# Kernel optimization log

Measured on AMD Instinct MI355X. Metric: run time of the kernel, lower is better.

Reference implementation:

```python
import jax, jax.numpy as jnp
import numpy as np

DN = ('NCHW', 'OIHW', 'NCHW')
EPS = 1e-5

def _conv(x, w, stride, padding):
    return jax.lax.conv_general_dilated(x, w, stride, padding, dimension_numbers=DN)

def _bn(x, g, b, m, v):
    # inference-mode BatchNorm2d
    s = g * jax.lax.rsqrt(v + EPS)
    return x * s[None, :, None, None] + (b - m * s)[None, :, None, None]

def _gn(x, g, b, groups):
    B, C, H, W = x.shape
    xr = x.reshape(B, groups, -1)
    mu = xr.mean(axis=2, keepdims=True)
    var = xr.var(axis=2, keepdims=True)
    xn = ((xr - mu) * jax.lax.rsqrt(var + EPS)).reshape(B, C, H, W)
    return xn * g[None, :, None, None] + b[None, :, None, None]

def _dsconv(f, ow, ob, og, obb, om, ov, w, wb, gg, gb, morph, k=3, extend_scope=1.0):
    B, C, H, W = f.shape
    S = H  # source DSC coordinate map only type-checks for square inputs
    off = jnp.tanh(_bn(_conv(f, ow, (1, 1), [(1, 1), (1, 1)]) + ob[None, :, None, None], og, obb, om, ov))
    # source passes y_offset for morph 0, x_offset for morph 1; both are added to y_new
    sel = off[:, :k] if morph == 0 else off[:, k:]
    center = k // 2
    # _apply_offset: detached clone, center zeroed; cumulative loop is empty for k=3
    off_cum = jax.lax.stop_gradient(sel).at[:, center].set(0.0) * extend_scope
    vals = jnp.linspace(float((-k) // 2), float(k // 2), k, dtype=f.dtype)  # [-2,-0.5,1] for k=3 (source quirk)
    rowc = jnp.arange(S, dtype=f.dtype)[:, None]  # both y_center and x_center equal the row index
    yg = jnp.zeros((k,), f.dtype) if morph == 0 else vals
    xg = vals if morph == 0 else jnp.zeros((k,), f.dtype)
    y = rowc[None, None] + yg[None, :, None, None] + off_cum                       # (B,k,S,S)
    x = jnp.broadcast_to(rowc[None, None] + xg[None, :, None, None], (B, k, S, S))
    rs = lambda t: t.transpose(0, 2, 1, 3).reshape(B, k * S, S)  # b p w h -> b (w p) h
    y, x = rs(y), rs(x)
    y0 = jnp.clip(jnp.floor(y), 0, S - 1); y1 = jnp.clip(jnp.floor(y) + 1.0, 0, S - 1)
    x0 = jnp.clip(jnp.floor(x), 0, S - 1); x1 = jnp.clip(jnp.floor(x) + 1.0, 0, S - 1)
    # source: index_a0 = base_y0 - base + x0  (batch offset cancels -> all batches gather from batch 0)
    flat0 = f[0].transpose(1, 2, 0).reshape(S * S, C)
    gat = lambda yy, xx: flat0[(yy * S + xx).astype(jnp.int32)]  # (B,kS,S,C)
    out = (gat(y0, x0) * ((y1 - y) * (x1 - x))[..., None]
         + gat(y0, x1) * ((y1 - y) * (x - x0))[..., None]
         + gat(y1, x0) * ((y - y0) * (x1 - x))[..., None]
         + gat(y1, x1) * ((y - y0) * (x - x0))[..., None])
    if morph == 0:
        df = out.transpose(0, 3, 1, 2)                    # (B,C,k*S,S)
        z = _conv(df, w, (k, 1), 'VALID')
    else:
        df = out.reshape(B, S, k * S, C).transpose(0, 3, 1, 2)  # (B,C,S,k*S)
        z = _conv(df, w, (1, k), 'VALID')
    z = z + wb[None, :, None, None]
    return jax.nn.silu(_gn(z, gg, gb, w.shape[0] // 4))

def _forward(x, w0, g0, b0, m0, v0,
             owx, obx, ogx, obbx, omx, ovx, wx, bwx, ggx, gbx,
             owy, oby, ogy, obby, omy, ovy, wy, bwy, ggy, gby):
    out0 = jax.nn.silu(_bn(_conv(x, w0, (1, 1), [(1, 1), (1, 1)]), g0, b0, m0, v0))
    outx = _dsconv(x, owx, obx, ogx, obbx, omx, ovx, wx, bwx, ggx, gbx, morph=0)
    outy = _dsconv(x, owy, oby, ogy, obby, omy, ovy, wy, bwy, ggy, gby, morph=1)
    return jnp.concatenate([out0, outx, outy], axis=1)

def setup_inputs() -> dict:
    B, C, O, S, K = 4, 64, 64, 256, 3
    key = jax.random.key(0)
    ks = jax.random.split(key, 32)
    rn = lambda i, sh, sc=1.0: jax.random.normal(ks[i], sh, dtype=jnp.float32) * sc
    ru = lambda i, sh: jax.random.uniform(ks[i], sh, dtype=jnp.float32) + 0.5
    return {
        'x': rn(0, (B, C, S, S)),
        'w0': rn(1, (O, C, 3, 3), 0.05), 'g0': ru(2, (O,)), 'b0': rn(3, (O,), 0.1),
        'm0': rn(4, (O,), 0.1), 'v0': ru(5, (O,)),
        'owx': rn(6, (2 * K, C, 3, 3), 0.05), 'obx': rn(7, (2 * K,), 0.1),
        'ogx': ru(8, (2 * K,)), 'obbx': rn(9, (2 * K,), 0.1), 'omx': rn(10, (2 * K,), 0.1), 'ovx': ru(11, (2 * K,)),
        'wx': rn(12, (O, C, K, 1), 0.05), 'bwx': rn(13, (O,), 0.1), 'ggx': ru(14, (O,)), 'gbx': rn(15, (O,), 0.1),
        'owy': rn(16, (2 * K, C, 3, 3), 0.05), 'oby': rn(17, (2 * K,), 0.1),
        'ogy': ru(18, (2 * K,)), 'obby': rn(19, (2 * K,), 0.1), 'omy': rn(20, (2 * K,), 0.1), 'ovy': ru(21, (2 * K,)),
        'wy': rn(22, (O, C, 1, K), 0.05), 'bwy': rn(23, (O,), 0.1), 'ggy': ru(24, (O,)), 'gby': rn(25, (O,), 0.1),
    }

def reference(x, w0, g0, b0, m0, v0,
              owx, obx, ogx, obbx, omx, ovx, wx, bwx, ggx, gbx,
              owy, oby, ogy, obby, omy, ovy, wy, bwy, ggy, gby):
    return _forward(x, w0, g0, b0, m0, v0,
                    owx, obx, ogx, obbx, omx, ovx, wx, bwx, ggx, gbx,
                    owy, oby, ogy, obby, omy, ovy, wy, bwy, ggy, gby)
```

## Files before the change

### kernel.cpp

```cpp
#include <hip/hip_runtime.h>
#include <hip/hip_bf16.h>
#include <math.h>

#define TS 256
#define HW 65536
#define CIN 64
#define EPSV 1e-5f
#define XPITCH 258

typedef __attribute__((ext_vector_type(8))) short bf16x8;
typedef __attribute__((ext_vector_type(4))) float f32x4;
typedef __attribute__((ext_vector_type(16))) float f32x16;
typedef __attribute__((ext_vector_type(4))) unsigned short u16x4;
typedef unsigned short ushort_t;

__device__ __forceinline__ float silu_f(float v){ return v / (1.0f + expf(-v)); }
__device__ __forceinline__ ushort_t f2bf(float f){
    __hip_bfloat16 h = __float2bfloat16(f);
    return *reinterpret_cast<ushort_t*>(&h);
}
__device__ __forceinline__ float bf2f(ushort_t u){
    unsigned int t = ((unsigned int)u) << 16;
    return __uint_as_float(t);
}

__global__ __launch_bounds__(256) void k_xbf(const float* __restrict__ x, ushort_t* __restrict__ xbf){
    int blk = blockIdx.x;
    int tid = threadIdx.x;
    if (blk < 4096){
        __shared__ float tile[64][65];
        int b = blk >> 10;
        int chunk = blk & 1023;
        int p0 = chunk * 64;
        int i = p0 >> 8, jb = p0 & 255;
        int lane = tid & 63, grp = tid >> 6;
        #pragma unroll
        for (int k = 0; k < 16; ++k){
            int c = k*4 + grp;
            tile[lane][c] = x[((size_t)(b*CIN + c))*HW + p0 + lane];
        }
        __syncthreads();
        #pragma unroll
        for (int k = 0; k < 16; ++k){
            int pp = k*4 + grp;
            xbf[(((size_t)b*258 + (i+1))*XPITCH + 1 + jb + pp)*64 + lane] = f2bf(tile[pp][lane]);
        }
    } else {
        int base = (blk - 4096) * 1024;
        #pragma unroll
        for (int k = 0; k < 4; ++k){
            int h = base + k*256 + tid;
            if (h < 132096){
                int b = h / 33024;
                int rem = h - b*33024;
                int r = (rem >= 16512) ? 257 : 0;
                int e = (rem >= 16512) ? rem - 16512 : rem;
                xbf[((size_t)b*258 + r)*XPITCH*64 + e] = 0;
            } else if (h < 263168){
                int h2 = h - 132096;
                int b = h2 >> 15;
                int rem = h2 & 32767;
                int row = rem >> 7;
                int rem2 = rem & 127;
                int colsel = rem2 >> 6;
                int c = rem2 & 63;
                xbf[(((size_t)b*258 + row + 1)*XPITCH + (colsel ? 257 : 0))*64 + c] = 0;
            }
        }
    }
}

__global__ __launch_bounds__(256) void k_wpack(const float* __restrict__ w0,
        const float* __restrict__ wx, const float* __restrict__ wy,
        ushort_t* __restrict__ w0bf, ushort_t* __restrict__ wbfx, ushort_t* __restrict__ wbfy){
    int idx = blockIdx.x*256 + threadIdx.x;
    if (idx < 36864){
        int r = idx >> 12;
        int rem = idx & 4095;
        int o = rem >> 6, c = rem & 63;
        w0bf[idx] = f2bf(w0[(o*64 + c)*9 + r]);
    } else {
        int k2 = idx - 36864;
        int set = k2 / 12288;
        int rem = k2 - set*12288;
        int o = rem / 192;
        int k = rem - o*192;
        int t = k >> 6, c = k & 63;
        const float* w = set ? wy : wx;
        ushort_t* dst = set ? wbfy : wbfx;
        dst[rem] = f2bf(w[(o*64 + c)*3 + t]);
    }
}

__global__ __launch_bounds__(256) void k_offp(const float* __restrict__ x,
        const float* __restrict__ owx, const float* __restrict__ owy,
        float* __restrict__ poff){
    __shared__ float xs[8][4][258];
    __shared__ float wsm[4][8][9];
    int by = blockIdx.y;
    int b = by >> 3, chunk = by & 7;
    int i0 = blockIdx.x * 2;
    int tid = threadIdx.x;
    for (int idx = tid; idx < 4*8*9; idx += 256){
        int o = idx / 72;
        int rem = idx - o*72;
        int c = rem / 9, tap = rem - c*9;
        int morph = o >> 1;
        int ch = (o==0)?0:(o==1)?2:(o==2)?3:5;
        const float* w = morph ? owy : owx;
        wsm[o][c][tap] = w[(ch*64 + chunk*8 + c)*9 + tap];
    }
    for (int idx = tid; idx < 8*4*258; idx += 256){
        int c = idx / 1032;
        int rem = idx - c*1032;
        int rr = rem / 258, col = rem - rr*258;
        int gy = i0 + rr - 1, gx = col - 1;
        float v = 0.f;
        if (gy >= 0 && gy < 256 && gx >= 0 && gx < 256)
            v = x[((size_t)(b*64 + chunk*8 + c))*HW + gy*256 + gx];
        xs[c][rr][col] = v;
    }
    __syncthreads();
    float acc[4][2];
    #pragma unroll
    for (int o = 0; o < 4; ++o){ acc[o][0]=0.f; acc[o][1]=0.f; }
    int j = tid;
    #pragma unroll
    for (int c = 0; c < 8; ++c){
        float vrow[4][3];
        #pragma unroll
        for (int rr = 0; rr < 4; ++rr){
            vrow[rr][0] = xs[c][rr][j];
            vrow[rr][1] = xs[c][rr][j+1];
            vrow[rr][2] = xs[c][rr][j+2];
        }
        #pragma unroll
        for (int o = 0; o < 4; ++o){
            const float* wr = wsm[o][c];
            #pragma unroll
            for (int ky = 0; ky < 3; ++ky){
                #pragma unroll
                for (int kx = 0; kx < 3; ++kx){
                    float wv = wr[ky*3+kx];
                    acc[o][0] += wv * vrow[ky][kx];
                    acc[o][1] += wv * vrow[ky+1][kx];
                }
            }
        }
    }
    #pragma unroll
    for (int o = 0; o < 4; ++o){
        size_t base = ((size_t)((chunk*4 + o)*4 + b))*HW;
        poff[base + (size_t)i0*256 + j]     = acc[o][0];
        poff[base + (size_t)(i0+1)*256 + j] = acc[o][1];
    }
}

__global__ __launch_bounds__(256) void k_mid(
        const ushort_t* __restrict__ xbf, const ushort_t* __restrict__ w0bf,
        const float* __restrict__ g0, const float* __restrict__ b0,
        const float* __restrict__ m0, const float* __restrict__ v0,
        const float* __restrict__ poff,
        const float* __restrict__ ogx, const float* __restrict__ ovx,
        const float* __restrict__ obx, const float* __restrict__ omx,
        const float* __restrict__ obbx,
        const float* __restrict__ ogy, const float* __restrict__ ovy,
        const float* __restrict__ oby, const float* __restrict__ omy,
        const float* __restrict__ obby,
        float* __restrict__ off0, float* __restrict__ off1,
        float* __restrict__ out){
    __shared__ __align__(16) ushort_t Xs[3*130*64];
    int blk = blockIdx.x;
    int tid = threadIdx.x;
    if (blk < 2048){
        int id2 = ((blk & 7) << 8) + (blk >> 3);
        int b  = id2 >> 9;
        int i  = (id2 >> 1) & 255;
        int jh = id2 & 1;
        int j0h = jh*128;
        int wv = tid >> 6;
        int lane = tid & 63;
        int l31 = lane & 31;
        int kh = lane >> 5;
        int obase = (wv & 1) * 32;
        int pxb = (wv >> 1) * 64;

        for (int idx = tid; idx < 3120; idx += 256){
            int rr = idx / 1040;
            int rem = idx - rr*1040;
            int p = rem >> 3, cgrp = rem & 7;
            bf16x8 v = *(const bf16x8*)(xbf + (((size_t)b*258 + (i + rr))*XPITCH + j0h + p)*64 + cgrp*8);
            int byte = rr*16640 + p*128 + ((cgrp*16) ^ ((p & 7) << 4));
            *(bf16x8*)((char*)Xs + byte) = v;
        }
        __syncthreads();

        f32x16 acc0, acc1;
        #pragma unroll
        for (int e = 0; e < 16; ++e){ acc0[e] = 0.f; acc1[e] = 0.f; }

        #pragma unroll
        for (int r = 0; r < 9; ++r){
            const int rr = r/3, dx = r%3 - 1;
            bf16x8 af[4];
            #pragma unroll
            for (int kg = 0; kg < 4; ++kg)
                af[kg] = *(const bf16x8*)(w0bf + (size_t)r*4096 + (obase + l31)*64 + kg*16 + kh*8);
            #pragma unroll
            for (int kg = 0; kg < 4; ++kg){
                int cb = kg*32 + kh*16;
                int p0_ = pxb + l31 + dx + 1;
                bf16x8 b0_ = *(const bf16x8*)((char*)Xs + rr*16640 + p0_*128 + (cb ^ ((p0_ & 7) << 4)));
                acc0 = __builtin_amdgcn_mfma_f32_32x32x16_bf16(af[kg], b0_, acc0, 0, 0, 0);
                int p1_ = p0_ + 32;
                bf16x8 b1_ = *(const bf16x8*)((char*)Xs + rr*16640 + p1_*128 + (cb ^ ((p1_ & 7) << 4)));
                acc1 = __builtin_amdgcn_mfma_f32_32x32x16_bf16(af[kg], b1_, acc1, 0, 0, 0);
            }
        }
        #pragma unroll
        for (int reg = 0; reg < 16; ++reg){
            int o = obase + (reg & 3) + 8*(reg >> 2) + 4*kh;
            float s = g0[o] * rsqrtf(v0[o] + EPSV);
            float bi = b0[o] - m0[o]*s;
            int j = j0h + pxb + l31;
            out[((size_t)(b*192 + o))*HW + i*TS + j]      = silu_f(acc0[reg]*s + bi);
            out[((size_t)(b*192 + o))*HW + i*TS + j + 32] = silu_f(acc1[reg]*s + bi);
        }
    } else {
        int idx = (blk - 2048)*256 + tid;
        int px = idx & 65535;
        int t2 = idx >> 16;
        int b = t2 & 3;
        int o6 = t2 >> 2;
        float s_ = 0.f;
        #pragma unroll
        for (int chunk = 0; chunk < 8; ++chunk)
            s_ += poff[((size_t)((chunk*4 + o6)*4 + b))*HW + px];
        int morph = o6 >> 1;
        int ch = (o6==0)?0:(o6==1)?2:(o6==2)?3:5;
        const float* og_ = morph? ogy:ogx; const float* ov_ = morph? ovy:ovx;
        const float* ob_ = morph? oby:obx; const float* om_ = morph? omy:omx;
        const float* obb_ = morph? obby:obbx;
        float sc = og_[ch]*rsqrtf(ov_[ch]+EPSV);
        float bi = (ob_[ch]-om_[ch])*sc + obb_[ch];
        int pl = (o6 & 1)*2;
        float* dst = (morph? off1:off0) + ((size_t)(b*3+pl))*HW;
        dst[px] = tanhf(s_*sc + bi);
    }
}

__global__ __launch_bounds__(256) void k_dsc2m(const ushort_t* __restrict__ xbf,
        const float* __restrict__ off0, const float* __restrict__ off1,
        const ushort_t* __restrict__ wbfx, const ushort_t* __restrict__ wbfy,
        const float* __restrict__ bwx, const float* __restrict__ bwy,
        ushort_t* __restrict__ zbuf, float* __restrict__ part){
    __shared__ __align__(16) ushort_t Vt[3*64*64];
    __shared__ __align__(16) ushort_t Xg[7][4][64];
    int mz = blockIdx.z;
    int b = mz & 3;
    int morph = mz >> 2;
    int i = blockIdx.y;
    int j0 = blockIdx.x * 64;
    int tid = threadIdx.x;
    int lane16 = tid & 15;
    int pq = tid >> 4;
    const float fi = (float)i;
    const float* offm = morph ? off1 : off0;

    if (morph == 0){
        int vec = tid >> 4;
        int s = vec >> 2, cs = vec & 3;
        int row = min(max(i - 1 + s, 0), 255);
        int col = min(max(i - 2 + cs, 0), 255);
        *(u16x4*)&Xg[s][cs][lane16*4] =
            *(const u16x4*)(xbf + ((size_t)(row+1)*XPITCH + 1 + col)*64 + lane16*4);
    } else {
        if (tid < 112){
            int s = tid >> 4;
            int row = min(max(i - 3 + s, 0), 255);
            *(u16x4*)&Xg[s][0][lane16*4] =
                *(const u16x4*)(xbf + ((size_t)(row+1)*XPITCH + 1 + i)*64 + lane16*4);
        }
    }
    __syncthreads();

    #pragma unroll
    for (int it = 0; it < 12; ++it){
        int pair = it*16 + pq;
        int t = pair >> 6, jloc = pair & 63;
        float y, wx1, wx0;
        int x0i, x1i;
        if (morph == 0){
            int j = j0 + jloc;
            float off = (t == 1) ? 0.f : offm[((size_t)(b*3 + t)*TS + i)*TS + j];
            y = fi + off;
            float vp = (t==0) ? -2.0f : ((t==1) ? -0.5f : 1.0f);
            float xf = fi + vp;
            float x0 = fminf(fmaxf(floorf(xf), 0.f), 255.f);
            float x1 = fminf(fmaxf(floorf(xf) + 1.f, 0.f), 255.f);
            wx1 = x1 - xf; wx0 = xf - x0;
            x0i = (int)x0; x1i = (int)x1;
        } else {
            int q = 3*(j0 + jloc) + t;
            int dl = q >> 8, jj = q & 255;
            float off = (dl == 1) ? 0.f : offm[((size_t)(b*3 + dl)*TS + i)*TS + jj];
            float vp = (dl==0) ? -2.0f : ((dl==1) ? -0.5f : 1.0f);
            y = fi + vp + off;
            wx1 = (i < 255) ? 1.f : 0.f; wx0 = 0.f;
            x0i = i; x1i = i;
        }
        float yf = floorf(y);
        float y0 = fminf(fmaxf(yf, 0.f), 255.f);
        float y1 = fminf(fmaxf(yf + 1.f, 0.f), 255.f);
        float wy1 = y1 - y, wy0 = y - y0;
        int y0i = (int)y0, y1i = (int)y1;
        int c0 = lane16*4;
        int rbase = morph ? (i - 3) : (i - 1);
        int rs0 = y0i - rbase;
        int rs1 = y1i - rbase;
        int cs0 = morph ? 0 : (x0i - (i - 2));
        u16x4 a  = *(const u16x4*)&Xg[rs0][cs0][c0];
        u16x4 c_ = *(const u16x4*)&Xg[rs1][cs0][c0];
        float v[4];
        if (morph == 0 && wx0 != 0.f){
            int cs1 = x1i - (i - 2);
            u16x4 bv = *(const u16x4*)&Xg[rs0][cs1][c0];
            u16x4 d  = *(const u16x4*)&Xg[rs1][cs1][c0];
            #pragma unroll
            for (int k = 0; k < 4; ++k)
                v[k] = wy1*(wx1*bf2f(a[k]) + wx0*bf2f(bv[k]))
                     + wy0*(wx1*bf2f(c_[k]) + wx0*bf2f(d[k]));
        } else {
            #pragma unroll
            for (int k = 0; k < 4; ++k)
                v[k] = wx1*(wy1*bf2f(a[k]) + wy0*bf2f(c_[k]));
        }
        unsigned int lo = (unsigned int)f2bf(v[0]) | ((unsigned int)f2bf(v[1]) << 16);
        unsigned int hi = (unsigned int)f2bf(v[2]) | ((unsigned int)f2bf(v[3]) << 16);
        int cbyte = (c0*2) ^ ((jloc & 7) << 4);
        uint2 pk; pk.x = lo; pk.y = hi;
        *(uint2*)((char*)Vt + t*8192 + jloc*128 + cbyte) = pk;
    }
    __syncthreads();

    const ushort_t* wbf = morph ? wbfy : wbfx;
    const float* wb = morph ? bwy : bwx;
    ushort_t* zb = zbuf + (size_t)morph*4*64*HW;

    int wv = tid >> 6;
    int lane = tid & 63;
    int l15 = lane & 15, lhi = lane >> 4;
    int mi = wv;
    f32x4 acc[4];
    #pragma unroll
    for (int ni = 0; ni < 4; ++ni) acc[ni] = (f32x4){0.f,0.f,0.f,0.f};
    bf16x8 af[6];
    #pragma unroll
    for (int ks = 0; ks < 6; ++ks)
        af[ks] = *(const bf16x8*)(wbf + (mi*16 + l15)*192 + ks*32 + lhi*8);
    #pragma unroll
    for (int ks = 0; ks < 6; ++ks){
        int t = ks >> 1;
        int cbyte = ((ks & 1)*32 + lhi*8)*2;
        #pragma unroll
        for (int ni = 0; ni < 4; ++ni){
            int j = ni*16 + l15;
            bf16x8 bfr = *(const bf16x8*)((char*)Vt + t*8192 + j*128 + (cbyte ^ ((j & 7) << 4)));
            acc[ni] = __builtin_amdgcn_mfma_f32_16x16x32_bf16(af[ks], bfr, acc[ni], 0, 0, 0);
        }
    }
    float rsum[4], rsq[4];
    #pragma unroll
    for (int reg = 0; reg < 4; ++reg){
        int o = mi*16 + lhi*4 + reg;
        float bias = wb[o];
        float rs = 0.f, rq = 0.f;
        #pragma unroll
        for (int ni = 0; ni < 4; ++ni){
            int j = j0 + ni*16 + l15;
            float val = acc[ni][reg] + bias;
            zb[((size_t)b*64 + o)*HW + i*TS + j] = f2bf(val);
            rs += val; rq += val*val;
        }
        #pragma unroll
        for (int m = 1; m < 16; m <<= 1){
            rs += __shfl_xor(rs, m, 64);
            rq += __shfl_xor(rq, m, 64);
        }
        rsum[reg] = rs; rsq[reg] = rq;
    }
    if (l15 == 0){
        float ts = rsum[0]+rsum[1]+rsum[2]+rsum[3];
        float tq = rsq[0]+rsq[1]+rsq[2]+rsq[3];
        int g = mi*4 + lhi;
        size_t slot = (((size_t)(morph*4 + b)*16 + g)*1024) + (blockIdx.y*4 + blockIdx.x);
        part[slot*2]   = ts;
        part[slot*2+1] = tq;
    }
}

__global__ __launch_bounds__(256) void k_gnfinal2(const float* __restrict__ part, float* __restrict__ stats){
    int slot = blockIdx.x;
    float s = 0.f, q = 0.f;
    for (int k = threadIdx.x; k < 1024; k += 256){
        s += part[((size_t)slot*1024 + k)*2];
        q += part[((size_t)slot*1024 + k)*2 + 1];
    }
    #pragma unroll
    for (int d = 32; d > 0; d >>= 1){ s += __shfl_down(s, d, 64); q += __shfl_down(q, d, 64); }
    __shared__ float rs[4], rq[4];
    int lane = threadIdx.x & 63, wv = threadIdx.x >> 6;
    if (lane == 0){ rs[wv] = s; rq[wv] = q; }
    __syncthreads();
    if (threadIdx.x == 0){
        float S = rs[0]+rs[1]+rs[2]+rs[3];
        float Q = rq[0]+rq[1]+rq[2]+rq[3];
        float inv = 1.f/262144.f;
        float mean = S*inv;
        float var = Q*inv - mean*mean;
        stats[slot*2] = mean;
        stats[slot*2+1] = rsqrtf(var + EPSV);
    }
}

__global__ __launch_bounds__(256) void k_gnapply(float* __restrict__ dout, const ushort_t* __restrict__ zb,
        const float* __restrict__ stats,
        const float* __restrict__ ggx, const float* __restrict__ gbx,
        const float* __restrict__ ggy, const float* __restrict__ gby){
    int idx = blockIdx.x*256 + threadIdx.x;
    int pix4 = idx & 16383;
    int chb = idx >> 14;
    int ch = chb & 127;
    int b = chb >> 7;
    int m = ch >> 6;
    int cc = ch & 63;
    int g = cc >> 2;
    const float* gg = m ? ggy : ggx;
    const float* gb = m ? gby : gbx;
    int si = ((m*4 + b)*16 + g)*2;
    float mean = stats[si], rsig = stats[si+1];
    float sc = rsig * gg[cc];
    float bi = gb[cc] - mean*sc;
    u16x4 zv = *(const u16x4*)(zb + (((size_t)(m*4 + b)*64 + cc)*HW) + (size_t)pix4*4);
    float4 v;
    v.x = silu_f(bf2f(zv[0])*sc + bi);
    v.y = silu_f(bf2f(zv[1])*sc + bi);
    v.z = silu_f(bf2f(zv[2])*sc + bi);
    v.w = silu_f(bf2f(zv[3])*sc + bi);
    float4* ptr = (float4*)(dout + ((size_t)(b*192 + 64 + ch))*HW) + pix4;
    *ptr = v;
}

extern "C" void kernel_launch(void* const* d_in, const int* in_sizes, int n_in,
                              void* d_out, int out_size, void* d_ws, size_t ws_size,
                              hipStream_t stream){
    const float* x    = (const float*)d_in[0];
    const float* w0   = (const float*)d_in[1];
    const float* g0   = (const float*)d_in[2];
    const float* b0   = (const float*)d_in[3];
    const float* m0   = (const float*)d_in[4];
    const float* v0   = (const float*)d_in[5];
    const float* owx  = (const float*)d_in[6];
    const float* obx  = (const float*)d_in[7];
    const float* ogx  = (const float*)d_in[8];
    const float* obbx = (const float*)d_in[9];
    const float* omx  = (const float*)d_in[10];
    const float* ovx  = (const float*)d_in[11];
    const float* wx   = (const float*)d_in[12];
    const float* bwx  = (const float*)d_in[13];
    const float* ggx  = (const float*)d_in[14];
    const float* gbx  = (const float*)d_in[15];
    const float* owy  = (const float*)d_in[16];
    const float* oby  = (const float*)d_in[17];
    const float* ogy  = (const float*)d_in[18];
    const float* obby = (const float*)d_in[19];
    const float* omy  = (const float*)d_in[20];
    const float* ovy  = (const float*)d_in[21];
    const float* wy   = (const float*)d_in[22];
    const float* bwy  = (const float*)d_in[23];
    const float* ggy  = (const float*)d_in[24];
    const float* gby  = (const float*)d_in[25];

    float* out = (float*)d_out;
    ushort_t* xbf  = (ushort_t*)d_ws;
    ushort_t* w0bf = (ushort_t*)((char*)d_ws + 34078464);
    ushort_t* wbfx = (ushort_t*)((char*)d_ws + 34152192);
    ushort_t* wbfy = (ushort_t*)((char*)d_ws + 34176768);
    float* off0  = (float*)((char*)d_ws + 34201344);
    float* off1  = (float*)((char*)d_ws + 37347072);
    float* poff  = (float*)((char*)d_ws + 40492800);
    ushort_t* zbuf = (ushort_t*)((char*)d_ws + 40492800);
    float* part  = (float*)((char*)d_ws + 107601664);
    float* stats = (float*)((char*)d_ws + 108650240);
    (void)ws_size;

    k_xbf<<<4353, 256, 0, stream>>>(x, xbf);
    k_wpack<<<240, 256, 0, stream>>>(w0, wx, wy, w0bf, wbfx, wbfy);
    k_offp<<<dim3(128,32), 256, 0, stream>>>(x, owx, owy, poff);
    k_mid<<<6144, 256, 0, stream>>>(xbf, w0bf, g0, b0, m0, v0, poff,
        ogx, ovx, obx, omx, obbx,
        ogy, ovy, oby, omy, obby,
        off0, off1, out);
    k_dsc2m<<<dim3(4,256,8), 256, 0, stream>>>(xbf, off0, off1, wbfx, wbfy, bwx, bwy, zbuf, part);
    k_gnfinal2<<<128, 256, 0, stream>>>(part, stats);
    k_gnapply<<<32768, 256, 0, stream>>>(out, zbuf, stats, ggx, gbx, ggy, gby);
}
```

Baseline: 257.6 us.

## Fuse bf16 input packing into offset-conv kernel with chunked channel layout

Merges the fp32-to-bf16 padded-input conversion kernel into the offset partial-convolution kernel, so x is read from global memory once and the already staged shared tile is reused to emit bf16 values. The bf16 buffer changes from pixel-major with 64 channels per pixel to 8 planes of 8 channels each, so each thread writes one 16-byte vector. All consumers (the main conv and the gather kernel) and the halo-zeroing code are updated to the new indexing, and the workspace offsets are shifted. This removes one launch and one full pass over x. In exchange, downstream reads of 64 channels per pixel now touch 8 separate planes, which may reduce locality in the main conv loads.

```diff
diff --git a/kernel.cpp b/kernel.cpp
--- a/kernel.cpp
+++ b/kernel.cpp
@@ -24,26 +24,77 @@
     return __uint_as_float(t);
 }
 
-__global__ __launch_bounds__(256) void k_xbf(const float* __restrict__ x, ushort_t* __restrict__ xbf){
+__global__ __launch_bounds__(256) void k_pre(const float* __restrict__ x,
+        const float* __restrict__ owx, const float* __restrict__ owy,
+        float* __restrict__ poff, ushort_t* __restrict__ xbf){
     int blk = blockIdx.x;
     int tid = threadIdx.x;
     if (blk < 4096){
-        __shared__ float tile[64][65];
-        int b = blk >> 10;
-        int chunk = blk & 1023;
-        int p0 = chunk * 64;
-        int i = p0 >> 8, jb = p0 & 255;
-        int lane = tid & 63, grp = tid >> 6;
-        #pragma unroll
-        for (int k = 0; k < 16; ++k){
-            int c = k*4 + grp;
-            tile[lane][c] = x[((size_t)(b*CIN + c))*HW + p0 + lane];
+        __shared__ float xs[8][4][258];
+        __shared__ float wsm[4][8][9];
+        int by = blk & 31;
+        int b = by >> 3, chunk = by & 7;
+        int i0 = (blk >> 5) * 2;
+        for (int idx = tid; idx < 4*8*9; idx += 256){
+            int o = idx / 72;
+            int rem = idx - o*72;
+            int c = rem / 9, tap = rem - c*9;
+            int morph = o >> 1;
+            int ch = (o==0)?0:(o==1)?2:(o==2)?3:5;
+            const float* w = morph ? owy : owx;
+            wsm[o][c][tap] = w[(ch*64 + chunk*8 + c)*9 + tap];
+        }
+        for (int idx = tid; idx < 8*4*258; idx += 256){
+            int c = idx / 1032;
+            int rem = idx - c*1032;
+            int rr = rem / 258, col = rem - rr*258;
+            int gy = i0 + rr - 1, gx = col - 1;
+            float v = 0.f;
+            if (gy >= 0 && gy < 256 && gx >= 0 && gx < 256)
+                v = x[((size_t)(b*64 + chunk*8 + c))*HW + gy*256 + gx];
+            xs[c][rr][col] = v;
         }
         __syncthreads();
-        #pragma unroll
-        for (int k = 0; k < 16; ++k){
-            int pp = k*4 + grp;
-            xbf[(((size_t)b*258 + (i+1))*XPITCH + 1 + jb + pp)*64 + lane] = f2bf(tile[pp][lane]);
+        float acc[4][2];
+        #pragma unroll
+        for (int o = 0; o < 4; ++o){ acc[o][0]=0.f; acc[o][1]=0.f; }
+        int j = tid;
+        #pragma unroll
+        for (int c = 0; c < 8; ++c){
+            float vrow[4][3];
+            #pragma unroll
+            for (int rr = 0; rr < 4; ++rr){
+                vrow[rr][0] = xs[c][rr][j];
+                vrow[rr][1] = xs[c][rr][j+1];
+                vrow[rr][2] = xs[c][rr][j+2];
+            }
+            #pragma unroll
+            for (int o = 0; o < 4; ++o){
+                const float* wr = wsm[o][c];
+                #pragma unroll
+                for (int ky = 0; ky < 3; ++ky){
+                    #pragma unroll
+                    for (int kx = 0; kx < 3; ++kx){
+                        float wv = wr[ky*3+kx];
+                        acc[o][0] += wv * vrow[ky][kx];
+                        acc[o][1] += wv * vrow[ky+1][kx];
+                    }
+                }
+            }
+        }
+        #pragma unroll
+        for (int o = 0; o < 4; ++o){
+            size_t base = ((size_t)((chunk*4 + o)*4 + b))*HW;
+            poff[base + (size_t)i0*256 + j]     = acc[o][0];
+            poff[base + (size_t)(i0+1)*256 + j] = acc[o][1];
+        }
+        #pragma unroll
+        for (int r2 = 0; r2 < 2; ++r2){
+            bf16x8 pk;
+            #pragma unroll
+            for (int c = 0; c < 8; ++c)
+                pk[c] = (short)f2bf(xs[c][r2+1][j+1]);
+            *(bf16x8*)(xbf + ((((size_t)(b*8 + chunk)*258) + (i0 + r2 + 1))*XPITCH + 1 + j)*8) = pk;
         }
     } else {
         int base = (blk - 4096) * 1024;
@@ -51,20 +102,20 @@
         for (int k = 0; k < 4; ++k){
             int h = base + k*256 + tid;
             if (h < 132096){
-                int b = h / 33024;
-                int rem = h - b*33024;
-                int r = (rem >= 16512) ? 257 : 0;
-                int e = (rem >= 16512) ? rem - 16512 : rem;
-                xbf[((size_t)b*258 + r)*XPITCH*64 + e] = 0;
+                int plane = h / 4128;
+                int rem = h - plane*4128;
+                int r = (rem >= 2064) ? 257 : 0;
+                int e = (rem >= 2064) ? rem - 2064 : rem;
+                xbf[((size_t)plane*258 + r)*2064 + e] = 0;
             } else if (h < 263168){
                 int h2 = h - 132096;
-                int b = h2 >> 15;
-                int rem = h2 & 32767;
-                int row = rem >> 7;
-                int rem2 = rem & 127;
-                int colsel = rem2 >> 6;
-                int c = rem2 & 63;
-                xbf[(((size_t)b*258 + row + 1)*XPITCH + (colsel ? 257 : 0))*64 + c] = 0;
+                int plane = h2 >> 12;
+                int rem = h2 & 4095;
+                int row = rem >> 4;
+                int rem2 = rem & 15;
+                int colsel = rem2 >> 3;
+                int c = rem2 & 7;
+                xbf[(((size_t)plane*258 + row + 1)*XPITCH + (colsel ? 257 : 0))*8 + c] = 0;
             }
         }
     }
@@ -89,70 +140,6 @@
         const float* w = set ? wy : wx;
         ushort_t* dst = set ? wbfy : wbfx;
         dst[rem] = f2bf(w[(o*64 + c)*3 + t]);
-    }
-}
-
-__global__ __launch_bounds__(256) void k_offp(const float* __restrict__ x,
-        const float* __restrict__ owx, const float* __restrict__ owy,
-        float* __restrict__ poff){
-    __shared__ float xs[8][4][258];
-    __shared__ float wsm[4][8][9];
-    int by = blockIdx.y;
-    int b = by >> 3, chunk = by & 7;
-    int i0 = blockIdx.x * 2;
-    int tid = threadIdx.x;
-    for (int idx = tid; idx < 4*8*9; idx += 256){
-        int o = idx / 72;
-        int rem = idx - o*72;
-        int c = rem / 9, tap = rem - c*9;
-        int morph = o >> 1;
-        int ch = (o==0)?0:(o==1)?2:(o==2)?3:5;
-        const float* w = morph ? owy : owx;
-        wsm[o][c][tap] = w[(ch*64 + chunk*8 + c)*9 + tap];
-    }
-    for (int idx = tid; idx < 8*4*258; idx += 256){
-        int c = idx / 1032;
-        int rem = idx - c*1032;
-        int rr = rem / 258, col = rem - rr*258;
-        int gy = i0 + rr - 1, gx = col - 1;
-        float v = 0.f;
-        if (gy >= 0 && gy < 256 && gx >= 0 && gx < 256)
-            v = x[((size_t)(b*64 + chunk*8 + c))*HW + gy*256 + gx];
-        xs[c][rr][col] = v;
-    }
-    __syncthreads();
-    float acc[4][2];
-    #pragma unroll
-    for (int o = 0; o < 4; ++o){ acc[o][0]=0.f; acc[o][1]=0.f; }
-    int j = tid;
-    #pragma unroll
-    for (int c = 0; c < 8; ++c){
-        float vrow[4][3];
-        #pragma unroll
-        for (int rr = 0; rr < 4; ++rr){
-            vrow[rr][0] = xs[c][rr][j];
-            vrow[rr][1] = xs[c][rr][j+1];
-            vrow[rr][2] = xs[c][rr][j+2];
-        }
-        #pragma unroll
-        for (int o = 0; o < 4; ++o){
-            const float* wr = wsm[o][c];
-            #pragma unroll
-            for (int ky = 0; ky < 3; ++ky){
-                #pragma unroll
-                for (int kx = 0; kx < 3; ++kx){
-                    float wv = wr[ky*3+kx];
-                    acc[o][0] += wv * vrow[ky][kx];
-                    acc[o][1] += wv * vrow[ky+1][kx];
-                }
-            }
-        }
-    }
-    #pragma unroll
-    for (int o = 0; o < 4; ++o){
-        size_t base = ((size_t)((chunk*4 + o)*4 + b))*HW;
-        poff[base + (size_t)i0*256 + j]     = acc[o][0];
-        poff[base + (size_t)(i0+1)*256 + j] = acc[o][1];
     }
 }
 
@@ -189,7 +176,7 @@
             int rr = idx / 1040;
             int rem = idx - rr*1040;
             int p = rem >> 3, cgrp = rem & 7;
-            bf16x8 v = *(const bf16x8*)(xbf + (((size_t)b*258 + (i + rr))*XPITCH + j0h + p)*64 + cgrp*8);
+            bf16x8 v = *(const bf16x8*)(xbf + ((((size_t)(b*8 + cgrp)*258) + (i + rr))*XPITCH + j0h + p)*8);
             int byte = rr*16640 + p*128 + ((cgrp*16) ^ ((p & 7) << 4));
             *(bf16x8*)((char*)Xs + byte) = v;
         }
@@ -272,14 +259,16 @@
         int s = vec >> 2, cs = vec & 3;
         int row = min(max(i - 1 + s, 0), 255);
         int col = min(max(i - 2 + cs, 0), 255);
+        int chunk = lane16 >> 1, off8 = (lane16 & 1)*4;
         *(u16x4*)&Xg[s][cs][lane16*4] =
-            *(const u16x4*)(xbf + ((size_t)(row+1)*XPITCH + 1 + col)*64 + lane16*4);
+            *(const u16x4*)(xbf + (((size_t)chunk*258 + row + 1)*XPITCH + 1 + col)*8 + off8);
     } else {
         if (tid < 112){
             int s = tid >> 4;
             int row = min(max(i - 3 + s, 0), 255);
+            int chunk = lane16 >> 1, off8 = (lane16 & 1)*4;
             *(u16x4*)&Xg[s][0][lane16*4] =
-                *(const u16x4*)(xbf + ((size_t)(row+1)*XPITCH + 1 + i)*64 + lane16*4);
+                *(const u16x4*)(xbf + (((size_t)chunk*258 + row + 1)*XPITCH + 1 + i)*8 + off8);
         }
     }
     __syncthreads();
@@ -483,20 +472,19 @@
 
     float* out = (float*)d_out;
     ushort_t* xbf  = (ushort_t*)d_ws;
-    ushort_t* w0bf = (ushort_t*)((char*)d_ws + 34078464);
-    ushort_t* wbfx = (ushort_t*)((char*)d_ws + 34152192);
-    ushort_t* wbfy = (ushort_t*)((char*)d_ws + 34176768);
-    float* off0  = (float*)((char*)d_ws + 34201344);
-    float* off1  = (float*)((char*)d_ws + 37347072);
-    float* poff  = (float*)((char*)d_ws + 40492800);
-    ushort_t* zbuf = (ushort_t*)((char*)d_ws + 40492800);
-    float* part  = (float*)((char*)d_ws + 107601664);
-    float* stats = (float*)((char*)d_ws + 108650240);
+    ushort_t* w0bf = (ushort_t*)((char*)d_ws + 34080768);
+    ushort_t* wbfx = (ushort_t*)((char*)d_ws + 34154496);
+    ushort_t* wbfy = (ushort_t*)((char*)d_ws + 34179072);
+    float* off0  = (float*)((char*)d_ws + 34203648);
+    float* off1  = (float*)((char*)d_ws + 37349376);
+    float* poff  = (float*)((char*)d_ws + 40495104);
+    ushort_t* zbuf = (ushort_t*)((char*)d_ws + 40495104);
+    float* part  = (float*)((char*)d_ws + 107603968);
+    float* stats = (float*)((char*)d_ws + 108652544);
     (void)ws_size;
 
-    k_xbf<<<4353, 256, 0, stream>>>(x, xbf);
+    k_pre<<<4353, 256, 0, stream>>>(x, owx, owy, poff, xbf);
     k_wpack<<<240, 256, 0, stream>>>(w0, wx, wy, w0bf, wbfx, wbfy);
-    k_offp<<<dim3(128,32), 256, 0, stream>>>(x, owx, owy, poff);
     k_mid<<<6144, 256, 0, stream>>>(xbf, w0bf, g0, b0, m0, v0, poff,
         ogx, ovx, obx, omx, obbx,
         ogy, ovy, oby, omy, obby,
```

After: 275.4 us. +6.9%, slower.
